# Kernel tuning notes

Measured on AMD Instinct MI355X. Metric: run time of the kernel, lower is better.

Reference implementation:

```python
import jax, jax.numpy as jnp
import numpy as np
from jax import lax

D_MODEL = 128   # C
D_STATE = 16    # n
D_CONV = 4
D_INNER = 256   # expand * d_model
DT_RANK = 8     # ceil(d_model / 16)
BATCH, HH, WW, DD = 1, 32, 32, 32


def _mk_mamba_params(key):
    ks = jax.random.split(key, 6)
    s = 0.02
    inW = jax.random.normal(ks[0], (2 * D_INNER, D_MODEL)) * s
    convw = jax.random.normal(ks[1], (D_INNER, D_CONV)) * 0.1
    convb = jnp.zeros((D_INNER,), jnp.float32)
    xpW = jax.random.normal(ks[2], (DT_RANK + 2 * D_STATE, D_INNER)) * s
    dtW = jax.random.normal(ks[3], (D_INNER, DT_RANK)) * s
    dtb = jax.random.normal(ks[4], (D_INNER,)) * 0.1
    Alog = jnp.log(jnp.tile(jnp.arange(1, D_STATE + 1, dtype=jnp.float32), (D_INNER, 1)))
    Dp = jnp.ones((D_INNER,), jnp.float32)
    outW = jax.random.normal(ks[5], (D_MODEL, D_INNER)) * s
    return inW, convw, convb, xpW, dtW, dtb, Alog, Dp, outW


def setup_inputs() -> dict:
    key = jax.random.key(0)
    kx, kv, kh, kd, kf = jax.random.split(key, 5)
    inp = {"x": jax.random.normal(kx, (BATCH, HH, WW, DD, D_MODEL), jnp.float32)}
    for tag, kk in (("v", kv), ("h", kh), ("d", kd)):
        inW, convw, convb, xpW, dtW, dtb, Alog, Dp, outW = _mk_mamba_params(kk)
        inp[f"inW_{tag}"] = inW
        inp[f"convw_{tag}"] = convw
        inp[f"convb_{tag}"] = convb
        inp[f"xpW_{tag}"] = xpW
        inp[f"dtW_{tag}"] = dtW
        inp[f"dtb_{tag}"] = dtb
        inp[f"Alog_{tag}"] = Alog
        inp[f"Dp_{tag}"] = Dp
        inp[f"outW_{tag}"] = outW
    kf1, kf2 = jax.random.split(kf)
    inp["fcW"] = jax.random.normal(kf1, (D_MODEL, 3 * D_MODEL)) * 0.02
    inp["fcb"] = jnp.zeros((D_MODEL,), jnp.float32)
    return inp


def _mamba(x, inW, convw, convb, xpW, dtW, dtb, Alog, Dp, outW):
    # x: (N, L, d_model)
    N, L, _ = x.shape
    xz = x @ inW.T                               # (N, L, 2*d_inner)
    xi, z = jnp.split(xz, 2, axis=-1)
    # depthwise causal conv1d (left-pad d_conv-1, cross-correlation like torch)
    xp = jnp.pad(xi, ((0, 0), (D_CONV - 1, 0), (0, 0)))
    xc = convb + sum(convw[:, k] * lax.dynamic_slice_in_dim(xp, k, L, 1) for k in range(D_CONV))
    xc = jax.nn.silu(xc)                         # (N, L, d_inner)
    dbc = xc @ xpW.T                             # (N, L, dt_rank + 2*n)
    dt, Bm, Cm = jnp.split(dbc, [DT_RANK, DT_RANK + D_STATE], axis=-1)
    dt = jax.nn.softplus(dt @ dtW.T + dtb)       # (N, L, d_inner)
    A = -jnp.exp(Alog)                           # (d_inner, n)

    def step(h, inp):
        dt_t, B_t, C_t, u_t = inp                # (N,d_in),(N,n),(N,n),(N,d_in)
        dA = jnp.exp(dt_t[:, :, None] * A)       # (N, d_inner, n)
        h = dA * h + (dt_t * u_t)[:, :, None] * B_t[:, None, :]
        y = jnp.einsum('bdn,bn->bd', h, C_t)
        return h, y

    h0 = jnp.zeros((N, D_INNER, D_STATE), x.dtype)
    xs = (jnp.swapaxes(dt, 0, 1), jnp.swapaxes(Bm, 0, 1),
          jnp.swapaxes(Cm, 0, 1), jnp.swapaxes(xc, 0, 1))
    _, ys = lax.scan(step, h0, xs)
    y = jnp.swapaxes(ys, 0, 1) + xc * Dp
    y = y * jax.nn.silu(z)
    return y @ outW.T                            # (N, L, d_model)


def reference(x,
              inW_v, convw_v, convb_v, xpW_v, dtW_v, dtb_v, Alog_v, Dp_v, outW_v,
              inW_h, convw_h, convb_h, xpW_h, dtW_h, dtb_h, Alog_h, Dp_h, outW_h,
              inW_d, convw_d, convb_d, xpW_d, dtW_d, dtb_d, Alog_d, Dp_d, outW_d,
              fcW, fcb):
    B, H, W, D, C = x.shape
    # vertical: scan over H
    v = jnp.transpose(x, (0, 2, 3, 1, 4)).reshape(-1, H, C)
    v = _mamba(v, inW_v, convw_v, convb_v, xpW_v, dtW_v, dtb_v, Alog_v, Dp_v, outW_v)
    v = jnp.transpose(v.reshape(B, W, D, H, C), (0, 3, 1, 2, 4))
    # horizontal: scan over W
    h = jnp.transpose(x, (0, 1, 3, 2, 4)).reshape(-1, W, C)
    h = _mamba(h, inW_h, convw_h, convb_h, xpW_h, dtW_h, dtb_h, Alog_h, Dp_h, outW_h)
    h = jnp.transpose(h.reshape(B, H, D, W, C), (0, 1, 3, 2, 4))
    # depth: scan over D
    d = x.reshape(-1, D, C)
    d = _mamba(d, inW_d, convw_d, convb_d, xpW_d, dtW_d, dtb_d, Alog_d, Dp_d, outW_d)
    d = d.reshape(B, H, W, D, C)
    out = jnp.concatenate([v, h, d], axis=-1)
    return out @ fcW.T + fcb
```

## Files before the change

### kernel.cpp

```cpp
#include <hip/hip_runtime.h>


#define XC_S 260
#define DBC_S 40
#define NPOS 32768

typedef __attribute__((ext_vector_type(8))) short bf16x8;
typedef __attribute__((ext_vector_type(16))) float f32x16;

struct InArgs {
  const float* __restrict__ x;
  const float* __restrict__ convw0; const float* __restrict__ convb0;
  const float* __restrict__ convw1; const float* __restrict__ convb1;
  const float* __restrict__ convw2; const float* __restrict__ convb2;
  const unsigned short* __restrict__ WBh;
  const unsigned short* __restrict__ WBl;
  const unsigned short* __restrict__ XPh;
  const unsigned short* __restrict__ XPl;
  const float* __restrict__ dtW0; const float* __restrict__ dtb0; const float* __restrict__ Dp0;
  const float* __restrict__ dtW1; const float* __restrict__ dtb1; const float* __restrict__ Dp1;
  const float* __restrict__ dtW2; const float* __restrict__ dtb2; const float* __restrict__ Dp2;
  float* __restrict__ y;
};

struct OutArgs {
  const unsigned* __restrict__ y;
  const unsigned short* __restrict__ MtH;
  const unsigned short* __restrict__ MtL;
  const float* __restrict__ fcb;
  float* __restrict__ out;
};

__device__ __forceinline__ float sigmoidf_(float v) {
  return 1.0f / (1.0f + __expf(-v));
}

__device__ __forceinline__ short bf16_rne_(float f) {
  unsigned u = __float_as_uint(f);
  unsigned r = u + 0x7fffu + ((u >> 16) & 1u);
  return (short)(r >> 16);
}

__device__ __forceinline__ float bf16_tof_(short h) {
  return __uint_as_float(((unsigned)(unsigned short)h) << 16);
}

__device__ __forceinline__ unsigned pack_hl_(float v) {
  unsigned u = __float_as_uint(v);
  unsigned hb = (u + 0x7fffu + ((u >> 16) & 1u)) & 0xffff0000u;
  float d = v - __uint_as_float(hb);
  return (hb >> 16) | (__float_as_uint(d) & 0xffff0000u);
}

__device__ __forceinline__ float unpack_hl_(unsigned p) {
  return __uint_as_float(p << 16) + __uint_as_float(p & 0xffff0000u);
}

__device__ __forceinline__ void unpack2_(uint4 a, uint4 b, bf16x8* hf, bf16x8* lf) {
  union { unsigned u[4]; bf16x8 v; } H, L;
  H.u[0] = (a.x & 0xffffu) | (a.y << 16);
  L.u[0] = (a.x >> 16)     | (a.y & 0xffff0000u);
  H.u[1] = (a.z & 0xffffu) | (a.w << 16);
  L.u[1] = (a.z >> 16)     | (a.w & 0xffff0000u);
  H.u[2] = (b.x & 0xffffu) | (b.y << 16);
  L.u[2] = (b.x >> 16)     | (b.y & 0xffff0000u);
  H.u[3] = (b.z & 0xffffu) | (b.w << 16);
  L.u[3] = (b.z >> 16)     | (b.w & 0xffff0000u);
  *hf = H.v; *lf = L.v;
}

extern "C" __global__ void __launch_bounds__(256)
mamba_prep(const float* __restrict__ fcW,
           const float* __restrict__ oWv, const float* __restrict__ oWh,
           const float* __restrict__ oWd,
           const float* __restrict__ iWv, const float* __restrict__ iWh,
           const float* __restrict__ iWd,
           const float* __restrict__ xpWv, const float* __restrict__ xpWh,
           const float* __restrict__ xpWd,
           unsigned short* __restrict__ MtH, unsigned short* __restrict__ MtL,
           unsigned short* __restrict__ WBh, unsigned short* __restrict__ WBl,
           unsigned short* __restrict__ XPH, unsigned short* __restrict__ XPL) {
  int bid = blockIdx.x;
  int j = threadIdx.x;
  if (bid < 384) {
    int br = bid >> 7, c = bid & 127;
    const float* oW = (br == 0) ? oWv : (br == 1) ? oWh : oWd;
    const float* fr = fcW + c * 384 + br * 128;
    float acc = 0.f;
    for (int m = 0; m < 128; ++m)
      acc = fmaf(fr[m], oW[m * 256 + j], acc);
    int st = br * 16 + (j >> 4), kh = (j >> 3) & 1, jj = j & 7;
    size_t idx = ((size_t)(st * 2 + kh) * 128 + c) * 8 + jj;
    short hi = bf16_rne_(acc);
    MtH[idx] = (unsigned short)hi;
    MtL[idx] = (unsigned short)bf16_rne_(acc - bf16_tof_(hi));
  } else if (bid < 768) {
    int b2 = bid - 384;
    int br = b2 >> 7, k = b2 & 127;
    const float* iW = (br == 0) ? iWv : (br == 1) ? iWh : iWd;
    int kg = k >> 3, kk = k & 7;
    size_t base = (size_t)br * 65536;

    float w0 = iW[j * 128 + k];
    short h0 = bf16_rne_(w0);
    size_t o0 = base + ((size_t)kg * 512 + j) * 8 + kk;
    WBh[o0] = (unsigned short)h0;
    WBl[o0] = (unsigned short)bf16_rne_(w0 - bf16_tof_(h0));

    float w1 = iW[(256 + j) * 128 + k];
    short h1 = bf16_rne_(w1);
    size_t o1 = base + ((size_t)kg * 512 + 256 + j) * 8 + kk;
    WBh[o1] = (unsigned short)h1;
    WBl[o1] = (unsigned short)bf16_rne_(w1 - bf16_tof_(h1));
  } else {
    int br = bid - 768;
    const float* xpW = (br == 0) ? xpWv : (br == 1) ? xpWh : xpWd;
    int k = j, st = k >> 4, kh = (k >> 3) & 1, jj = k & 7;
    for (int n = 0; n < 64; ++n) {
      float v = (n < 40) ? xpW[n * 256 + k] : 0.f;
      short hi = bf16_rne_(v);
      size_t idx = (size_t)br * 16384 + ((size_t)(st * 2 + kh) * 64 + n) * 8 + jj;
      XPH[idx] = (unsigned short)hi;
      XPL[idx] = (unsigned short)bf16_rne_(v - bf16_tof_(hi));
    }
  }
}

extern "C" __global__ void __launch_bounds__(256)
mamba_core(InArgs a) {
  __shared__ __align__(16) unsigned xiP[256 * 33];
  __shared__ __align__(16) float gS[256 * 33];
  __shared__ __align__(16) float dbcS[1280];

  const int tid = threadIdx.x;
  const int bid = blockIdx.x;
  const int br = bid >> 10;
  const int s  = bid & 1023;

  const int w = tid >> 6;
  const int lane = tid & 63;
  const int row = lane & 31;
  const int kh = lane >> 5;

  const float* convw = (br == 0) ? a.convw0 : (br == 1) ? a.convw1 : a.convw2;
  const float* convb = (br == 0) ? a.convb0 : (br == 1) ? a.convb1 : a.convb2;
  const unsigned short* WH = a.WBh + br * 65536;
  const unsigned short* WL = a.WBl + br * 65536;

  int xst;
  if (br == 0) xst = 131072; else if (br == 1) xst = 4096; else xst = 128;
  int i0 = s >> 5, i1 = s & 31;
  int xbase;
  if (br == 0)      xbase = i0*4096   + i1*128;
  else if (br == 1) xbase = i0*131072 + i1*128;
  else              xbase = i0*131072 + i1*4096;

  const float* xrow = a.x + xbase + (size_t)row * xst;
  bf16x8 ah[8], al[8];
  #pragma unroll
  for (int st = 0; st < 8; ++st) {
    const float* xp = xrow + st * 16 + kh * 8;
    float4 f0 = *(const float4*)&xp[0];
    float4 f1 = *(const float4*)&xp[4];
    float fs[8] = {f0.x, f0.y, f0.z, f0.w, f1.x, f1.y, f1.z, f1.w};
    #pragma unroll
    for (int jj = 0; jj < 8; ++jj) {
      unsigned u = __float_as_uint(fs[jj]);
      unsigned hb = (u + 0x7fffu + ((u >> 16) & 1u)) & 0xffff0000u;
      ah[st][jj] = (short)(hb >> 16);
      al[st][jj] = (short)(__float_as_uint(fs[jj] - __uint_as_float(hb)) >> 16);
    }
  }

  const bool is_xi = (w < 2);

  #pragma unroll 1
  for (int j = 0; j < 4; ++j) {
    const int tl = w * 4 + j;
    const int col = tl * 32 + row;

    f32x16 acc0 = {0.f,0.f,0.f,0.f,0.f,0.f,0.f,0.f,
                   0.f,0.f,0.f,0.f,0.f,0.f,0.f,0.f};
    f32x16 acc1 = {0.f,0.f,0.f,0.f,0.f,0.f,0.f,0.f,
                   0.f,0.f,0.f,0.f,0.f,0.f,0.f,0.f};

    #pragma unroll
    for (int st = 0; st < 8; ++st) {
      const int kg = st * 2 + kh;
      const size_t boff = ((size_t)kg * 512 + col) * 8;
      bf16x8 bh = *(const bf16x8*)&WH[boff];
      bf16x8 bl = *(const bf16x8*)&WL[boff];
      if (st & 1) {
        acc1 = __builtin_amdgcn_mfma_f32_32x32x16_bf16(ah[st], bh, acc1, 0, 0, 0);
        acc1 = __builtin_amdgcn_mfma_f32_32x32x16_bf16(ah[st], bl, acc1, 0, 0, 0);
        acc1 = __builtin_amdgcn_mfma_f32_32x32x16_bf16(al[st], bh, acc1, 0, 0, 0);
      } else {
        acc0 = __builtin_amdgcn_mfma_f32_32x32x16_bf16(ah[st], bh, acc0, 0, 0, 0);
        acc0 = __builtin_amdgcn_mfma_f32_32x32x16_bf16(ah[st], bl, acc0, 0, 0, 0);
        acc0 = __builtin_amdgcn_mfma_f32_32x32x16_bf16(al[st], bh, acc0, 0, 0, 0);
      }
    }

    float av[16];
    #pragma unroll
    for (int i = 0; i < 16; ++i) av[i] = acc0[i] + acc1[i];

    if (is_xi) {
      float sw[16];
      #pragma unroll
      for (int i = 0; i < 16; ++i) sw[i] = __shfl_xor(av[i], 32);

      float4 cw = *(const float4*)&convw[col * 4];
      float cb = convb[col];

      #pragma unroll
      for (int i = 0; i < 16; ++i) {
        const int q = i >> 2;
        const int r0 = (i & 3) + 8 * q;
        float m1, m2, m3;
        if ((i & 3) == 0) {
          m1 = kh ? sw[4*q+3] : (q ? sw[4*q-1] : 0.f);
          m2 = kh ? sw[4*q+2] : (q ? sw[4*q-2] : 0.f);
          m3 = kh ? sw[4*q+1] : (q ? sw[4*q-3] : 0.f);
        } else if ((i & 3) == 1) {
          m1 = av[i-1];
          m2 = kh ? sw[4*q+3] : (q ? sw[4*q-1] : 0.f);
          m3 = kh ? sw[4*q+2] : (q ? sw[4*q-2] : 0.f);
        } else if ((i & 3) == 2) {
          m1 = av[i-1];
          m2 = av[i-2];
          m3 = kh ? sw[4*q+3] : (q ? sw[4*q-1] : 0.f);
        } else {
          m1 = av[i-1];
          m2 = av[i-2];
          m3 = av[i-3];
        }
        float v = cb + cw.w * av[i] + cw.z * m1 + cw.y * m2 + cw.x * m3;
        v = v * sigmoidf_(v);
        const int t = r0 + 4 * kh;
        xiP[col * 33 + t] = pack_hl_(v);
      }
    } else {
      const int g0col = col - 256;
      #pragma unroll
      for (int i = 0; i < 16; ++i) {
        const int r = (i & 3) + 8 * (i >> 2) + 4 * kh;
        float zv = av[i];
        gS[g0col * 33 + r] = zv * sigmoidf_(zv);
      }
    }
  }

  const float* dtW = (br == 0) ? a.dtW0 : (br == 1) ? a.dtW1 : a.dtW2;
  const float* dtb = (br == 0) ? a.dtb0 : (br == 1) ? a.dtb1 : a.dtb2;
  const float* Dp  = (br == 0) ? a.Dp0  : (br == 1) ? a.Dp1  : a.Dp2;
  const int d = tid;
  float4 wA0 = *(const float4*)&dtW[d * 8];
  float4 wA1 = *(const float4*)&dtW[d * 8 + 4];
  float biasA = dtb[d];
  float DpA = Dp[d];

  __syncthreads();

  const int u0 = d * 33;
  unsigned uPn = xiP[u0];
  float gAn = gS[u0];

  if (w < 2) {
    const unsigned short* XH = a.XPh + br * 16384;
    const unsigned short* XL = a.XPl + br * 16384;
    f32x16 g0 = {0.f,0.f,0.f,0.f,0.f,0.f,0.f,0.f,
                 0.f,0.f,0.f,0.f,0.f,0.f,0.f,0.f};
    f32x16 g1 = {0.f,0.f,0.f,0.f,0.f,0.f,0.f,0.f,
                 0.f,0.f,0.f,0.f,0.f,0.f,0.f,0.f};
    #pragma unroll
    for (int st = 0; st < 16; ++st) {
      const int kg = st * 2 + kh;
      const int base2 = kg * 264 + row;
      unsigned e0 = xiP[base2];
      unsigned e1 = xiP[base2 + 33];
      unsigned e2 = xiP[base2 + 66];
      unsigned e3 = xiP[base2 + 99];
      unsigned e4 = xiP[base2 + 132];
      unsigned e5 = xiP[base2 + 165];
      unsigned e6 = xiP[base2 + 198];
      unsigned e7 = xiP[base2 + 231];
      union { unsigned u[4]; bf16x8 v; } H, L;
      H.u[0] = (e0 & 0xffffu) | (e1 << 16);
      L.u[0] = (e0 >> 16)     | (e1 & 0xffff0000u);
      H.u[1] = (e2 & 0xffffu) | (e3 << 16);
      L.u[1] = (e2 >> 16)     | (e3 & 0xffff0000u);
      H.u[2] = (e4 & 0xffffu) | (e5 << 16);
      L.u[2] = (e4 >> 16)     | (e5 & 0xffff0000u);
      H.u[3] = (e6 & 0xffffu) | (e7 << 16);
      L.u[3] = (e6 >> 16)     | (e7 & 0xffff0000u);
      bf16x8 ahf = H.v, alf = L.v;
      const size_t bo = ((size_t)kg * 64 + w * 32 + row) * 8;
      bf16x8 bh = *(const bf16x8*)&XH[bo];
      bf16x8 bl = *(const bf16x8*)&XL[bo];
      if (st & 1) {
        g1 = __builtin_amdgcn_mfma_f32_32x32x16_bf16(ahf, bh, g1, 0, 0, 0);
        g1 = __builtin_amdgcn_mfma_f32_32x32x16_bf16(ahf, bl, g1, 0, 0, 0);
        g1 = __builtin_amdgcn_mfma_f32_32x32x16_bf16(alf, bh, g1, 0, 0, 0);
      } else {
        g0 = __builtin_amdgcn_mfma_f32_32x32x16_bf16(ahf, bh, g0, 0, 0, 0);
        g0 = __builtin_amdgcn_mfma_f32_32x32x16_bf16(ahf, bl, g0, 0, 0, 0);
        g0 = __builtin_amdgcn_mfma_f32_32x32x16_bf16(alf, bh, g0, 0, 0, 0);
      }
    }
    const int ncol = w * 32 + row;
    if (ncol < 40) {
      #pragma unroll
      for (int i = 0; i < 16; ++i) {
        const int t = (i & 3) + 8 * (i >> 2) + 4 * kh;
        dbcS[t * DBC_S + ncol] = g0[i] + g1[i];
      }
    }
  }

  __syncthreads();

  unsigned* yG = (unsigned*)(a.y + (size_t)(br * 1024 + s) * 8192);

  float hsA[16];
  #pragma unroll
  for (int n = 0; n < 16; ++n) hsA[n] = 0.f;

  float4 q0n = *(const float4*)&dbcS[0];
  float4 q1n = *(const float4*)&dbcS[4];
  float4 B0n = *(const float4*)&dbcS[8];
  float4 B1n = *(const float4*)&dbcS[12];

  #pragma unroll 1
  for (int t = 0; t < 32; ++t) {
    const int bb = t * DBC_S;
    float4 q0 = q0n, q1 = q1n, B0 = B0n, B1 = B1n;
    float gA = gAn;
    float uA = unpack_hl_(uPn);
    float4 B2 = *(const float4*)&dbcS[bb + 16];
    float4 B3 = *(const float4*)&dbcS[bb + 20];
    float4 C0 = *(const float4*)&dbcS[bb + 24];
    float4 C1 = *(const float4*)&dbcS[bb + 28];
    float4 C2 = *(const float4*)&dbcS[bb + 32];
    float4 C3 = *(const float4*)&dbcS[bb + 36];
    if (t < 31) {
      const int nb = bb + DBC_S;
      q0n = *(const float4*)&dbcS[nb];
      q1n = *(const float4*)&dbcS[nb + 4];
      B0n = *(const float4*)&dbcS[nb + 8];
      B1n = *(const float4*)&dbcS[nb + 12];
      uPn = xiP[u0 + t + 1];
      gAn = gS[u0 + t + 1];
    }

    float svA = biasA + q0.x*wA0.x + q0.y*wA0.y + q0.z*wA0.z + q0.w*wA0.w
                      + q1.x*wA1.x + q1.y*wA1.y + q1.z*wA1.z + q1.w*wA1.w;
    float dttA = fmaxf(svA, 0.f) + __logf(1.f + __expf(-fabsf(svA)));
    float coef = dttA * uA;
    float r1 = __expf(-dttA);
    float r8 = __expf(-8.f * dttA);
    float r2 = r1*r1,  r3 = r2*r1,  r4 = r2*r2;
    float r5 = r4*r1,  r6 = r4*r2,  r7 = r4*r3;
    float r9 = r8*r1,  r10 = r8*r2, r11 = r8*r3, r12 = r8*r4;
    float r13 = r8*r5, r14 = r8*r6, r15 = r8*r7, r16 = r8*r8;

    hsA[0]  = r1 *hsA[0]  + coef*B0.x;
    hsA[1]  = r2 *hsA[1]  + coef*B0.y;
    hsA[2]  = r3 *hsA[2]  + coef*B0.z;
    hsA[3]  = r4 *hsA[3]  + coef*B0.w;
    hsA[4]  = r5 *hsA[4]  + coef*B1.x;
    hsA[5]  = r6 *hsA[5]  + coef*B1.y;
    hsA[6]  = r7 *hsA[6]  + coef*B1.z;
    hsA[7]  = r8 *hsA[7]  + coef*B1.w;
    hsA[8]  = r9 *hsA[8]  + coef*B2.x;
    hsA[9]  = r10*hsA[9]  + coef*B2.y;
    hsA[10] = r11*hsA[10] + coef*B2.z;
    hsA[11] = r12*hsA[11] + coef*B2.w;
    hsA[12] = r13*hsA[12] + coef*B3.x;
    hsA[13] = r14*hsA[13] + coef*B3.y;
    hsA[14] = r15*hsA[14] + coef*B3.z;
    hsA[15] = r16*hsA[15] + coef*B3.w;

    float y0 = 0.f, y1 = 0.f, y2 = 0.f, y3 = 0.f;
    y0 += hsA[0] *C0.x;  y1 += hsA[1] *C0.y;
    y2 += hsA[2] *C0.z;  y3 += hsA[3] *C0.w;
    y0 += hsA[4] *C1.x;  y1 += hsA[5] *C1.y;
    y2 += hsA[6] *C1.z;  y3 += hsA[7] *C1.w;
    y0 += hsA[8] *C2.x;  y1 += hsA[9] *C2.y;
    y2 += hsA[10]*C2.z;  y3 += hsA[11]*C2.w;
    y0 += hsA[12]*C3.x;  y1 += hsA[13]*C3.y;
    y2 += hsA[14]*C3.z;  y3 += hsA[15]*C3.w;

    float ysA = (y0 + y1) + (y2 + y3);
    yG[t * 256 + d] = pack_hl_((ysA + uA * DpA) * gA);
  }
}

extern "C" __global__ void __launch_bounds__(256)
mamba_outproj(OutArgs a) {
  __shared__ __align__(16) unsigned ys[32 * XC_S];

  const int tid = threadIdx.x;
  const int b = blockIdx.x;
  const int p0 = b * 32;
  const int w = tid >> 6;
  const int lane = tid & 63;
  const int lam = lane & 31;
  const int kh = lane >> 5;
  const int col = w * 32 + lam;

  f32x16 g0 = {0.f,0.f,0.f,0.f,0.f,0.f,0.f,0.f,
               0.f,0.f,0.f,0.f,0.f,0.f,0.f,0.f};
  f32x16 g1 = {0.f,0.f,0.f,0.f,0.f,0.f,0.f,0.f,
               0.f,0.f,0.f,0.f,0.f,0.f,0.f,0.f};

  for (int br = 0; br < 3; ++br) {
    size_t base; int stride;
    if (br == 0) {
      int t = p0 >> 10, rem = p0 & 1023;
      base = ((size_t)rem) * 8192 + t * 256;              stride = 8192;
    } else if (br == 1) {
      int i0 = p0 >> 10, t = (p0 >> 5) & 31;
      base = ((size_t)(1024 + i0 * 32)) * 8192 + t * 256; stride = 8192;
    } else {
      int i0 = p0 >> 10, i1 = (p0 >> 5) & 31;
      base = ((size_t)(2048 + i0 * 32 + i1)) * 8192;      stride = 256;
    }
    __syncthreads();
    #pragma unroll
    for (int j = 0; j < 8; ++j) {
      int idx4 = tid + j * 256;
      int r = idx4 >> 6, c4 = idx4 & 63;
      *(uint4*)&ys[r * XC_S + c4 * 4] =
          *(const uint4*)&a.y[base + (size_t)r * stride + c4 * 4];
    }
    __syncthreads();

    #pragma unroll
    for (int stp = 0; stp < 16; ++stp) {
      const unsigned* ap = &ys[lam * XC_S + stp * 16 + kh * 8];
      uint4 ea = *(const uint4*)&ap[0];
      uint4 eb = *(const uint4*)&ap[4];
      bf16x8 ahf, alf;
      unpack2_(ea, eb, &ahf, &alf);
      const int st = br * 16 + stp;
      const size_t bidx = ((size_t)(st * 2 + kh) * 128 + col) * 8;
      bf16x8 bh = *(const bf16x8*)&a.MtH[bidx];
      bf16x8 bl = *(const bf16x8*)&a.MtL[bidx];
      if (stp & 1) {
        g1 = __builtin_amdgcn_mfma_f32_32x32x16_bf16(ahf, bh, g1, 0, 0, 0);
        g1 = __builtin_amdgcn_mfma_f32_32x32x16_bf16(ahf, bl, g1, 0, 0, 0);
        g1 = __builtin_amdgcn_mfma_f32_32x32x16_bf16(alf, bh, g1, 0, 0, 0);
      } else {
        g0 = __builtin_amdgcn_mfma_f32_32x32x16_bf16(ahf, bh, g0, 0, 0, 0);
        g0 = __builtin_amdgcn_mfma_f32_32x32x16_bf16(ahf, bl, g0, 0, 0, 0);
        g0 = __builtin_amdgcn_mfma_f32_32x32x16_bf16(alf, bh, g0, 0, 0, 0);
      }
    }
  }

  float fb = a.fcb[col];
  #pragma unroll
  for (int i = 0; i < 16; ++i) {
    const int r = (i & 3) + 8 * (i >> 2) + 4 * kh;
    a.out[(size_t)(p0 + r) * 128 + col] = g0[i] + g1[i] + fb;
  }
}

extern "C" void kernel_launch(void* const* d_in, const int* in_sizes, int n_in,
                              void* d_out, int out_size, void* d_ws, size_t ws_size,
                              hipStream_t stream) {
  const float* fcW = (const float*)d_in[28];
  const float* fcb = (const float*)d_in[29];

  unsigned short* MtH = (unsigned short*)d_ws;
  unsigned short* MtL = MtH + 98304;
  unsigned short* WBh = MtL + 98304;
  unsigned short* WBl = WBh + 3 * 65536;
  unsigned short* XPH = WBl + 3 * 65536;
  unsigned short* XPL = XPH + 3 * 16384;
  float* y    = (float*)(XPL + 3 * 16384);

  InArgs ia;
  ia.x = (const float*)d_in[0];
  ia.convw0 = (const float*)d_in[2];  ia.convb0 = (const float*)d_in[3];
  ia.convw1 = (const float*)d_in[11]; ia.convb1 = (const float*)d_in[12];
  ia.convw2 = (const float*)d_in[20]; ia.convb2 = (const float*)d_in[21];
  ia.WBh = WBh; ia.WBl = WBl;
  ia.XPh = XPH; ia.XPl = XPL;
  ia.dtW0 = (const float*)d_in[5];  ia.dtb0 = (const float*)d_in[6];  ia.Dp0 = (const float*)d_in[8];
  ia.dtW1 = (const float*)d_in[14]; ia.dtb1 = (const float*)d_in[15]; ia.Dp1 = (const float*)d_in[17];
  ia.dtW2 = (const float*)d_in[23]; ia.dtb2 = (const float*)d_in[24]; ia.Dp2 = (const float*)d_in[26];
  ia.y = y;

  OutArgs oa;
  oa.y = (const unsigned*)y; oa.MtH = MtH; oa.MtL = MtL;
  oa.fcb = fcb; oa.out = (float*)d_out;

  mamba_prep<<<771, 256, 0, stream>>>(
      fcW, (const float*)d_in[9], (const float*)d_in[18], (const float*)d_in[27],
      (const float*)d_in[1], (const float*)d_in[10], (const float*)d_in[19],
      (const float*)d_in[4], (const float*)d_in[13], (const float*)d_in[22],
      MtH, MtL, WBh, WBl, XPH, XPL);
  mamba_core<<<3072, 256, 0, stream>>>(ia);
  mamba_outproj<<<1024, 256, 0, stream>>>(oa);
}
```

Measured before the change: 396.8 us.

## Store scan outputs in position-major layout, split xproj K across warps, add accumulators

The core kernel now writes its scan outputs in a position-major layout, so the output projection reads one contiguous block per branch instead of strided rows. The x-projection MFMA now runs on all four warps: the K range is split in half into two shared-memory planes, which are then summed. The out-projection uses four independent accumulators and the prep GEMV four partial sums, both to shorten dependency chains. In exchange, the core kernel's stores become scattered across strides, and it adds an extra shared buffer and barrier.

New measurement: 373.1 us. 6.0% less time.

```diff
diff --git a/kernel.cpp b/kernel.cpp
--- a/kernel.cpp
+++ b/kernel.cpp
@@ -86,9 +86,14 @@
     int br = bid >> 7, c = bid & 127;
     const float* oW = (br == 0) ? oWv : (br == 1) ? oWh : oWd;
     const float* fr = fcW + c * 384 + br * 128;
-    float acc = 0.f;
-    for (int m = 0; m < 128; ++m)
-      acc = fmaf(fr[m], oW[m * 256 + j], acc);
+    float a0 = 0.f, a1 = 0.f, a2 = 0.f, a3 = 0.f;
+    for (int m = 0; m < 128; m += 4) {
+      a0 = fmaf(fr[m + 0], oW[(m + 0) * 256 + j], a0);
+      a1 = fmaf(fr[m + 1], oW[(m + 1) * 256 + j], a1);
+      a2 = fmaf(fr[m + 2], oW[(m + 2) * 256 + j], a2);
+      a3 = fmaf(fr[m + 3], oW[(m + 3) * 256 + j], a3);
+    }
+    float acc = (a0 + a1) + (a2 + a3);
     int st = br * 16 + (j >> 4), kh = (j >> 3) & 1, jj = j & 7;
     size_t idx = ((size_t)(st * 2 + kh) * 128 + c) * 8 + jj;
     short hi = bf16_rne_(acc);
@@ -131,6 +136,7 @@
   __shared__ __align__(16) unsigned xiP[256 * 33];
   __shared__ __align__(16) float gS[256 * 33];
   __shared__ __align__(16) float dbcS[1280];
+  __shared__ __align__(16) float dbcS2[1280];
 
   const int tid = threadIdx.x;
   const int bid = blockIdx.x;
@@ -266,15 +272,19 @@
   unsigned uPn = xiP[u0];
   float gAn = gS[u0];
 
-  if (w < 2) {
+  {
     const unsigned short* XH = a.XPh + br * 16384;
     const unsigned short* XL = a.XPl + br * 16384;
+    const int khalf = w >> 1;
+    const int ncol = (w & 1) * 32 + row;
+    float* plane = khalf ? dbcS2 : dbcS;
     f32x16 g0 = {0.f,0.f,0.f,0.f,0.f,0.f,0.f,0.f,
                  0.f,0.f,0.f,0.f,0.f,0.f,0.f,0.f};
     f32x16 g1 = {0.f,0.f,0.f,0.f,0.f,0.f,0.f,0.f,
                  0.f,0.f,0.f,0.f,0.f,0.f,0.f,0.f};
     #pragma unroll
-    for (int st = 0; st < 16; ++st) {
+    for (int st2 = 0; st2 < 8; ++st2) {
+      const int st = khalf * 8 + st2;
       const int kg = st * 2 + kh;
       const int base2 = kg * 264 + row;
       unsigned e0 = xiP[base2];
@@ -295,10 +305,10 @@
       H.u[3] = (e6 & 0xffffu) | (e7 << 16);
       L.u[3] = (e6 >> 16)     | (e7 & 0xffff0000u);
       bf16x8 ahf = H.v, alf = L.v;
-      const size_t bo = ((size_t)kg * 64 + w * 32 + row) * 8;
+      const size_t bo = ((size_t)kg * 64 + ncol) * 8;
       bf16x8 bh = *(const bf16x8*)&XH[bo];
       bf16x8 bl = *(const bf16x8*)&XL[bo];
-      if (st & 1) {
+      if (st2 & 1) {
         g1 = __builtin_amdgcn_mfma_f32_32x32x16_bf16(ahf, bh, g1, 0, 0, 0);
         g1 = __builtin_amdgcn_mfma_f32_32x32x16_bf16(ahf, bl, g1, 0, 0, 0);
         g1 = __builtin_amdgcn_mfma_f32_32x32x16_bf16(alf, bh, g1, 0, 0, 0);
@@ -308,19 +318,31 @@
         g0 = __builtin_amdgcn_mfma_f32_32x32x16_bf16(alf, bh, g0, 0, 0, 0);
       }
     }
-    const int ncol = w * 32 + row;
     if (ncol < 40) {
       #pragma unroll
       for (int i = 0; i < 16; ++i) {
         const int t = (i & 3) + 8 * (i >> 2) + 4 * kh;
-        dbcS[t * DBC_S + ncol] = g0[i] + g1[i];
+        plane[t * DBC_S + ncol] = g0[i] + g1[i];
       }
     }
   }
 
   __syncthreads();
 
-  unsigned* yG = (unsigned*)(a.y + (size_t)(br * 1024 + s) * 8192);
+  #pragma unroll
+  for (int i = 0; i < 5; ++i) {
+    int idx = tid + i * 256;
+    dbcS[idx] += dbcS2[idx];
+  }
+
+  __syncthreads();
+
+  unsigned* yG = (unsigned*)a.y + (size_t)br * (NPOS * 256);
+  int cbase, cstep;
+  if (br == 0)      { cbase = s * 256;                              cstep = 262144; }
+  else if (br == 1) { cbase = (s >> 5) * 262144 + (s & 31) * 256;   cstep = 8192; }
+  else              { cbase = s * 8192;                             cstep = 256; }
+  yG += cbase;
 
   float hsA[16];
   #pragma unroll
@@ -392,7 +414,7 @@
     y2 += hsA[14]*C3.z;  y3 += hsA[15]*C3.w;
 
     float ysA = (y0 + y1) + (y2 + y3);
-    yG[t * 256 + d] = pack_hl_((ysA + uA * DpA) * gA);
+    yG[t * cstep + d] = pack_hl_((ysA + uA * DpA) * gA);
   }
 }
 
@@ -411,28 +433,16 @@
 
   f32x16 g0 = {0.f,0.f,0.f,0.f,0.f,0.f,0.f,0.f,
                0.f,0.f,0.f,0.f,0.f,0.f,0.f,0.f};
-  f32x16 g1 = {0.f,0.f,0.f,0.f,0.f,0.f,0.f,0.f,
-               0.f,0.f,0.f,0.f,0.f,0.f,0.f,0.f};
+  f32x16 g1 = g0, g2 = g0, g3 = g0;
 
   for (int br = 0; br < 3; ++br) {
-    size_t base; int stride;
-    if (br == 0) {
-      int t = p0 >> 10, rem = p0 & 1023;
-      base = ((size_t)rem) * 8192 + t * 256;              stride = 8192;
-    } else if (br == 1) {
-      int i0 = p0 >> 10, t = (p0 >> 5) & 31;
-      base = ((size_t)(1024 + i0 * 32)) * 8192 + t * 256; stride = 8192;
-    } else {
-      int i0 = p0 >> 10, i1 = (p0 >> 5) & 31;
-      base = ((size_t)(2048 + i0 * 32 + i1)) * 8192;      stride = 256;
-    }
+    const uint4* src = (const uint4*)a.y + (((size_t)br * NPOS + p0) << 6);
     __syncthreads();
     #pragma unroll
     for (int j = 0; j < 8; ++j) {
       int idx4 = tid + j * 256;
       int r = idx4 >> 6, c4 = idx4 & 63;
-      *(uint4*)&ys[r * XC_S + c4 * 4] =
-          *(const uint4*)&a.y[base + (size_t)r * stride + c4 * 4];
+      *(uint4*)&ys[r * XC_S + c4 * 4] = src[idx4];
     }
     __syncthreads();
 
@@ -447,14 +457,22 @@
       const size_t bidx = ((size_t)(st * 2 + kh) * 128 + col) * 8;
       bf16x8 bh = *(const bf16x8*)&a.MtH[bidx];
       bf16x8 bl = *(const bf16x8*)&a.MtL[bidx];
-      if (stp & 1) {
+      if ((stp & 3) == 0) {
+        g0 = __builtin_amdgcn_mfma_f32_32x32x16_bf16(ahf, bh, g0, 0, 0, 0);
+        g0 = __builtin_amdgcn_mfma_f32_32x32x16_bf16(ahf, bl, g0, 0, 0, 0);
+        g0 = __builtin_amdgcn_mfma_f32_32x32x16_bf16(alf, bh, g0, 0, 0, 0);
+      } else if ((stp & 3) == 1) {
         g1 = __builtin_amdgcn_mfma_f32_32x32x16_bf16(ahf, bh, g1, 0, 0, 0);
         g1 = __builtin_amdgcn_mfma_f32_32x32x16_bf16(ahf, bl, g1, 0, 0, 0);
         g1 = __builtin_amdgcn_mfma_f32_32x32x16_bf16(alf, bh, g1, 0, 0, 0);
+      } else if ((stp & 3) == 2) {
+        g2 = __builtin_amdgcn_mfma_f32_32x32x16_bf16(ahf, bh, g2, 0, 0, 0);
+        g2 = __builtin_amdgcn_mfma_f32_32x32x16_bf16(ahf, bl, g2, 0, 0, 0);
+        g2 = __builtin_amdgcn_mfma_f32_32x32x16_bf16(alf, bh, g2, 0, 0, 0);
       } else {
-        g0 = __builtin_amdgcn_mfma_f32_32x32x16_bf16(ahf, bh, g0, 0, 0, 0);
-        g0 = __builtin_amdgcn_mfma_f32_32x32x16_bf16(ahf, bl, g0, 0, 0, 0);
-        g0 = __builtin_amdgcn_mfma_f32_32x32x16_bf16(alf, bh, g0, 0, 0, 0);
+        g3 = __builtin_amdgcn_mfma_f32_32x32x16_bf16(ahf, bh, g3, 0, 0, 0);
+        g3 = __builtin_amdgcn_mfma_f32_32x32x16_bf16(ahf, bl, g3, 0, 0, 0);
+        g3 = __builtin_amdgcn_mfma_f32_32x32x16_bf16(alf, bh, g3, 0, 0, 0);
       }
     }
   }
@@ -463,7 +481,7 @@
   #pragma unroll
   for (int i = 0; i < 16; ++i) {
     const int r = (i & 3) + 8 * (i >> 2) + 4 * kh;
-    a.out[(size_t)(p0 + r) * 128 + col] = g0[i] + g1[i] + fb;
+    a.out[(size_t)(p0 + r) * 128 + col] = (g0[i] + g1[i]) + (g2[i] + g3[i]) + fb;
   }
 }
 
```
